# Kernel tuning notes

Measured on AMD Instinct MI355X. Metric: run time of the kernel, lower is better.

## Reference

```python
import jax, jax.numpy as jnp
import numpy as np

N = 16383        # complete binary tree, 14 levels
D_NODE = 512
D_SSM = 512
D_STATE = 16
MAX_DEPTH = 14   # number of BFS levels (depth 0..13)
LN_EPS = 1e-5


def setup_inputs() -> dict:
    key = jax.random.key(0)
    ks = jax.random.split(key, 8)
    # tree structure: parent[i] = (i-1)//2, root has parent -1; BFS order == index order
    parent = np.concatenate([np.array([-1]), (np.arange(1, N) - 1) // 2]).astype(np.int64)
    depth = np.floor(np.log2(np.arange(N) + 1)).astype(np.int32)
    s = jax.random.normal(ks[0], (N, D_NODE), jnp.float32)
    w = jax.random.uniform(ks[1], (N,), jnp.float32, minval=0.01, maxval=1.0)
    # parameters (xavier-ish scales)
    W_in = jax.random.normal(ks[2], (D_SSM, D_NODE + 1), jnp.float32) * (1.0 / np.sqrt(D_NODE + 1))
    b_in = jnp.zeros((D_SSM,), jnp.float32)
    W_delta = jax.random.normal(ks[3], (D_SSM, D_SSM), jnp.float32) * (1.0 / np.sqrt(D_SSM))
    # dt-style bias init: softplus(b) ~ dt in [1e-3, 1e-1]
    dt = jnp.exp(jax.random.uniform(ks[4], (D_SSM,), jnp.float32) * (np.log(0.1) - np.log(0.001)) + np.log(0.001))
    b_delta = dt + jnp.log(-jnp.expm1(-dt))
    W_w = jax.random.normal(ks[5], (D_SSM, 1), jnp.float32)
    b_w = jnp.zeros((D_SSM,), jnp.float32)
    A_log = jnp.log(jnp.broadcast_to(jnp.arange(1.0, D_STATE + 1.0, dtype=jnp.float32)[None, :], (D_SSM, D_STATE)))
    D = jnp.ones((D_SSM,), jnp.float32)
    W_B = jax.random.normal(ks[6], (D_STATE, D_SSM), jnp.float32) * (1.0 / np.sqrt(D_SSM))
    b_B = jnp.zeros((D_STATE,), jnp.float32)
    W_C = jax.random.normal(ks[7], (D_STATE, D_SSM), jnp.float32) * (1.0 / np.sqrt(D_SSM))
    b_C = jnp.zeros((D_STATE,), jnp.float32)
    gamma = jnp.ones((D_SSM,), jnp.float32)
    beta = jnp.zeros((D_SSM,), jnp.float32)
    return {"s": s, "w": w, "parent": jnp.asarray(parent), "depth": jnp.asarray(depth),
            "W_in": W_in, "b_in": b_in, "W_delta": W_delta, "b_delta": b_delta,
            "W_w": W_w, "b_w": b_w, "A_log": A_log, "D": D,
            "W_B": W_B, "b_B": b_B, "W_C": W_C, "b_C": b_C,
            "gamma": gamma, "beta": beta}


def reference(s, w, parent, depth, W_in, b_in, W_delta, b_delta, W_w, b_w,
              A_log, D, W_B, b_B, W_C, b_C, gamma, beta):
    n = s.shape[0]
    log_w = jnp.log(w + 1e-6)[:, None]                       # [N, 1]
    feat = jnp.concatenate([s, log_w], axis=1)               # [N, d_node+1]
    x = feat @ W_in.T + b_in                                 # [N, d_ssm]
    delta = jax.nn.softplus(x @ W_delta.T + b_delta) * jax.nn.sigmoid(log_w @ W_w.T + b_w)  # [N, d_ssm]
    A = -jnp.exp(A_log)                                      # [d_ssm, d_state]
    B = x @ W_B.T + b_B                                      # [N, d_state]
    C = x @ W_C.T + b_C                                      # [N, d_state]
    A_bar = jnp.exp(delta[:, :, None] * A[None])             # [N, d_ssm, d_state]
    Bx = (delta * x)[:, :, None] * B[:, None, :]             # [N, d_ssm, d_state]
    # level-parallel tree scan: all nodes at BFS depth l updated together
    par = jnp.maximum(parent, 0)
    has_par = (parent >= 0)[:, None, None]
    H = jnp.zeros((n, A_bar.shape[1], A_bar.shape[2]), x.dtype)
    for lvl in range(MAX_DEPTH):
        h_par = jnp.where(has_par, jnp.take(H, par, axis=0), 0.0)
        H = jnp.where((depth == lvl)[:, None, None], A_bar * h_par + Bx, H)
    Y = jnp.einsum('nds,ns->nd', H, C) + D * x               # [N, d_ssm]
    mu = jnp.mean(Y, axis=-1, keepdims=True)
    var = jnp.var(Y, axis=-1, keepdims=True)
    return (Y - mu) / jnp.sqrt(var + LN_EPS) * gamma + beta
```

## Files before the change

### kernel.cpp

```cpp
#include <hip/hip_runtime.h>
#include <hip/hip_bf16.h>
#include <math.h>

#define D_SSM 512
#define D_STATE 16
#define CKPT_BASE 511
#define CKPT_END 1023
#define N_CKPT 512
#define MPAD 16384

typedef __attribute__((ext_vector_type(8))) short short8;
typedef __attribute__((ext_vector_type(4))) float floatx4;

__device__ __forceinline__ unsigned short f2bf(float f) {
    unsigned int u = __float_as_uint(f);
    unsigned int r = (u + 0x7fffu + ((u >> 16) & 1u)) >> 16;
    return (unsigned short)r;
}
__device__ __forceinline__ float bf2f(unsigned short u) {
    return __uint_as_float(((unsigned int)u) << 16);
}
__device__ __forceinline__ void g2lds16(const void* g, void* l) {
    __builtin_amdgcn_global_load_lds(
        (const __attribute__((address_space(1))) void*)g,
        (__attribute__((address_space(3))) void*)l, 16, 0, 0);
}

__global__ __launch_bounds__(256) void prep_kernel(
    const float* __restrict__ s, const float* __restrict__ w,
    const float* __restrict__ W_in, const float* __restrict__ W_delta,
    const float* __restrict__ W_B, const float* __restrict__ W_C,
    unsigned short* __restrict__ s_bf, float* __restrict__ lw,
    unsigned short* __restrict__ Win_bf, unsigned short* __restrict__ Wd_bf,
    unsigned short* __restrict__ Wbc_bf, int Nn)
{
    const int b = blockIdx.x, t = threadIdx.x;
    if (b < MPAD) {
        unsigned int pack = 0;
        if (b < Nn) {
            float2 sv = *(const float2*)(s + (size_t)b * 512 + t * 2);
            pack = (unsigned int)f2bf(sv.x) | ((unsigned int)f2bf(sv.y) << 16);
        }
        *(unsigned int*)(s_bf + (size_t)b * 512 + t * 2) = pack;
        if (t == 0) lw[b] = (b < Nn) ? logf(w[b] + 1e-6f) : 0.f;
    } else if (b < MPAD + 512) {
        int c = b - MPAD;
        float a0 = W_in[(size_t)c * 513 + t * 2];
        float a1 = W_in[(size_t)c * 513 + t * 2 + 1];
        *(unsigned int*)(Win_bf + (size_t)c * 512 + t * 2) =
            (unsigned int)f2bf(a0) | ((unsigned int)f2bf(a1) << 16);
    } else if (b < MPAD + 1024) {
        int c = b - MPAD - 512;
        float2 wv = *(const float2*)(W_delta + (size_t)c * 512 + t * 2);
        *(unsigned int*)(Wd_bf + (size_t)c * 512 + t * 2) =
            (unsigned int)f2bf(wv.x) | ((unsigned int)f2bf(wv.y) << 16);
    } else {
        int c = b - MPAD - 1024;
        const float* src = (c < 16) ? (W_B + (size_t)c * 512) : (W_C + (size_t)(c - 16) * 512);
        float2 wv = *(const float2*)(src + t * 2);
        *(unsigned int*)(Wbc_bf + (size_t)c * 512 + t * 2) =
            (unsigned int)f2bf(wv.x) | ((unsigned int)f2bf(wv.y) << 16);
    }
}

__global__ __launch_bounds__(256) void gemm_mfma(
    const unsigned short* __restrict__ Abf,
    const unsigned short* __restrict__ Wbf,
    float* __restrict__ outf,
    unsigned short* __restrict__ outbf,
    const float* __restrict__ bias,
    const float* __restrict__ lw,
    const float* __restrict__ wcol, int wcol_stride,
    const float* __restrict__ bw,
    int mode)
{
    __shared__ __align__(16) short As[2][64 * 32];
    __shared__ __align__(16) short Bs[2][128 * 32];
    const int tid = threadIdx.x;
    const int wave = tid >> 6, lane = tid & 63;
    const int row0 = blockIdx.y * 64;
    const int col0 = blockIdx.x * 128;
    const int wr = (wave >> 1) * 32;
    const int wc = (wave & 1) * 64;

    floatx4 acc[2][4] = {};

    const int srow = lane >> 2;
    const int sg   = (lane & 3) ^ ((srow >> 1) & 3);
    const int scol = sg * 8;

    const unsigned short* Ag = Abf + (size_t)(row0 + wave * 16 + srow) * 512 + scol;
    const unsigned short* Wg0 = Wbf + (size_t)(col0 + (wave * 2 + 0) * 16 + srow) * 512 + scol;
    const unsigned short* Wg1 = Wbf + (size_t)(col0 + (wave * 2 + 1) * 16 + srow) * 512 + scol;

    {
        g2lds16(Ag, (char*)&As[0][0] + wave * 1024);
        g2lds16(Wg0, (char*)&Bs[0][0] + (wave * 2 + 0) * 1024);
        g2lds16(Wg1, (char*)&Bs[0][0] + (wave * 2 + 1) * 1024);
    }
    __syncthreads();

    for (int it = 0; it < 16; it++) {
        const int cur = it & 1;
        if (it < 15) {
            int k1 = (it + 1) * 32;
            g2lds16(Ag + k1, (char*)&As[cur ^ 1][0] + wave * 1024);
            g2lds16(Wg0 + k1, (char*)&Bs[cur ^ 1][0] + (wave * 2 + 0) * 1024);
            g2lds16(Wg1 + k1, (char*)&Bs[cur ^ 1][0] + (wave * 2 + 1) * 1024);
        }

        short8 af[2], bfr[4];
        #pragma unroll
        for (int i = 0; i < 2; i++) {
            int m = wr + i * 16 + (lane & 15);
            int gm = (lane >> 4) ^ ((m >> 1) & 3);
            af[i] = *(const short8*)&As[cur][m * 32 + gm * 8];
        }
        #pragma unroll
        for (int j = 0; j < 4; j++) {
            int n = wc + j * 16 + (lane & 15);
            int gn = (lane >> 4) ^ ((n >> 1) & 3);
            bfr[j] = *(const short8*)&Bs[cur][n * 32 + gn * 8];
        }
        #pragma unroll
        for (int i = 0; i < 2; i++)
            #pragma unroll
            for (int j = 0; j < 4; j++)
                acc[i][j] = __builtin_amdgcn_mfma_f32_16x16x32_bf16(af[i], bfr[j], acc[i][j], 0, 0, 0);
        __syncthreads();
    }

    #pragma unroll
    for (int i = 0; i < 2; i++) {
        #pragma unroll
        for (int reg = 0; reg < 4; reg++) {
            int r = row0 + wr + i * 16 + (lane >> 4) * 4 + reg;
            float lwr = lw[r];
            #pragma unroll
            for (int j = 0; j < 4; j++) {
                int c = col0 + wc + j * 16 + (lane & 15);
                float z = acc[i][j][reg] + bias[c];
                if (mode == 0) {
                    float o = z + lwr * wcol[(size_t)c * wcol_stride];
                    outbf[(size_t)r * 512 + c] = f2bf(o);
                } else {
                    float sp = (z > 15.f) ? z : log1pf(__expf(z));
                    float sg2 = 1.f / (1.f + __expf(-(lwr * wcol[c] + bw[c])));
                    outf[(size_t)r * 512 + c] = sp * sg2;
                }
            }
        }
    }
}

__global__ __launch_bounds__(256) void bc_gemm(
    const unsigned short* __restrict__ Abf,
    const unsigned short* __restrict__ Wbc,
    const float* __restrict__ b_B, const float* __restrict__ b_C,
    float* __restrict__ Bm, float* __restrict__ Cm)
{
    __shared__ __align__(16) short As[128 * 32];
    __shared__ __align__(16) short Ws[32 * 512];
    const int tid = threadIdx.x;
    const int wave = tid >> 6, lane = tid & 63;
    const int row0 = blockIdx.x * 128;
    const int wr = wave * 32;

    for (int i = 0; i < 8; i++) {
        int fg = i * 256 + tid;
        int n = fg >> 6, kgg = fg & 63;
        short8 v = *(const short8*)(Wbc + (size_t)n * 512 + kgg * 8);
        *(short8*)&Ws[n * 512 + ((kgg ^ (n & 7)) * 8)] = v;
    }

    floatx4 acc[2][2] = {};

    const int srow = lane >> 2;
    const int sgz  = (lane & 3) ^ ((srow >> 1) & 3);
    const int scol = sgz * 8;

    for (int k0 = 0; k0 < 512; k0 += 32) {
        #pragma unroll
        for (int j = 0; j < 2; j++) {
            int c = wave * 2 + j;
            int r = c * 16 + srow;
            g2lds16(Abf + (size_t)(row0 + r) * 512 + k0 + scol, (char*)As + c * 1024);
        }
        __syncthreads();

        short8 af[2], bfr[2];
        #pragma unroll
        for (int i = 0; i < 2; i++) {
            int m = wr + i * 16 + (lane & 15);
            int gm = (lane >> 4) ^ ((m >> 1) & 3);
            af[i] = *(const short8*)&As[m * 32 + gm * 8];
        }
        #pragma unroll
        for (int j = 0; j < 2; j++) {
            int n = j * 16 + (lane & 15);
            int Gg = (k0 >> 3) + (lane >> 4);
            bfr[j] = *(const short8*)&Ws[n * 512 + ((Gg ^ (n & 7)) * 8)];
        }
        #pragma unroll
        for (int i = 0; i < 2; i++)
            #pragma unroll
            for (int j = 0; j < 2; j++)
                acc[i][j] = __builtin_amdgcn_mfma_f32_16x16x32_bf16(af[i], bfr[j], acc[i][j], 0, 0, 0);
        __syncthreads();
    }

    const int s = lane & 15;
    #pragma unroll
    for (int i = 0; i < 2; i++) {
        #pragma unroll
        for (int reg = 0; reg < 4; reg++) {
            int r = row0 + wr + i * 16 + (lane >> 4) * 4 + reg;
            Bm[(size_t)r * 16 + s] = acc[i][0][reg] + b_B[s];
            Cm[(size_t)r * 16 + s] = acc[i][1][reg] + b_C[s];
        }
    }
}

__device__ __forceinline__ bool geo_check(const float* As) {
    bool ok = true;
    #pragma unroll
    for (int s = 1; s < 16; s++) {
        float want = (float)(s + 1) * As[0];
        ok = ok && (fabsf(As[s] - want) <= 1e-4f * (float)(s + 1));
    }
    return ok;
}

__global__ __launch_bounds__(256) void ckpt_kernel(
    const unsigned short* __restrict__ x_bf, const float* __restrict__ delta,
    const float* __restrict__ Bm, const float* __restrict__ A_log,
    float* __restrict__ H9)
{
    const int n9 = blockIdx.x;
    const int t = threadIdx.x;
    const int d0 = t, d1 = t + 256;

    float As0[16], As1[16], acc0[16], acc1[16];
    #pragma unroll
    for (int s = 0; s < 16; s++) {
        As0[s] = -__expf(A_log[d0 * 16 + s]);
        As1[s] = -__expf(A_log[d1 * 16 + s]);
        acc0[s] = 0.f; acc1[s] = 0.f;
    }
    const bool fast = geo_check(As0) && geo_check(As1);

    float cum0 = 0.f, cum1 = 0.f;
    int a = CKPT_BASE + n9;
    while (a >= 0) {
        float da0 = delta[(size_t)a * 512 + d0];
        float da1 = delta[(size_t)a * 512 + d1];
        float bx0 = da0 * bf2f(x_bf[(size_t)a * 512 + d0]);
        float bx1 = da1 * bf2f(x_bf[(size_t)a * 512 + d1]);
        if (fast) {
            float r0 = __expf(As0[0] * cum0);
            float r1 = __expf(As1[0] * cum1);
            float pw0 = r0, pw1 = r1;
            #pragma unroll
            for (int s = 0; s < 16; s++) {
                float Bs = Bm[a * 16 + s];
                acc0[s] = fmaf(bx0 * pw0, Bs, acc0[s]);
                acc1[s] = fmaf(bx1 * pw1, Bs, acc1[s]);
                pw0 *= r0; pw1 *= r1;
            }
        } else {
            #pragma unroll
            for (int s = 0; s < 16; s++) {
                float Bs = Bm[a * 16 + s];
                acc0[s] = fmaf(bx0 * __expf(As0[s] * cum0), Bs, acc0[s]);
                acc1[s] = fmaf(bx1 * __expf(As1[s] * cum1), Bs, acc1[s]);
            }
        }
        cum0 += da0; cum1 += da1;
        a = (a - 1) >> 1;
    }

    float* p0 = H9 + ((size_t)n9 * 512 + d0) * 16;
    float* p1 = H9 + ((size_t)n9 * 512 + d1) * 16;
    #pragma unroll
    for (int s = 0; s < 16; s++) { p0[s] = acc0[s]; p1[s] = acc1[s]; }
}

__global__ __launch_bounds__(256) void scan_shallow(
    const unsigned short* __restrict__ x_bf, const float* __restrict__ delta,
    const float* __restrict__ Bm, const float* __restrict__ Cm,
    const float* __restrict__ A_log, const float* __restrict__ Dv,
    const float* __restrict__ gamma, const float* __restrict__ beta,
    float* __restrict__ out)
{
    const int n = blockIdx.x;
    const int t = threadIdx.x;
    const int d0 = t, d1 = t + 256;

    float As0[16], As1[16], acc0[16], acc1[16];
    #pragma unroll
    for (int s = 0; s < 16; s++) {
        As0[s] = -__expf(A_log[d0 * 16 + s]);
        As1[s] = -__expf(A_log[d1 * 16 + s]);
        acc0[s] = 0.f; acc1[s] = 0.f;
    }
    const bool fast = geo_check(As0) && geo_check(As1);

    float cum0 = 0.f, cum1 = 0.f;
    int a = n;
    while (a >= 0) {
        float da0 = delta[(size_t)a * 512 + d0];
        float da1 = delta[(size_t)a * 512 + d1];
        float bx0 = da0 * bf2f(x_bf[(size_t)a * 512 + d0]);
        float bx1 = da1 * bf2f(x_bf[(size_t)a * 512 + d1]);
        if (fast) {
            float r0 = __expf(As0[0] * cum0);
            float r1 = __expf(As1[0] * cum1);
            float pw0 = r0, pw1 = r1;
            #pragma unroll
            for (int s = 0; s < 16; s++) {
                float Bs = Bm[a * 16 + s];
                acc0[s] = fmaf(bx0 * pw0, Bs, acc0[s]);
                acc1[s] = fmaf(bx1 * pw1, Bs, acc1[s]);
                pw0 *= r0; pw1 *= r1;
            }
        } else {
            #pragma unroll
            for (int s = 0; s < 16; s++) {
                float Bs = Bm[a * 16 + s];
                acc0[s] = fmaf(bx0 * __expf(As0[s] * cum0), Bs, acc0[s]);
                acc1[s] = fmaf(bx1 * __expf(As1[s] * cum1), Bs, acc1[s]);
            }
        }
        cum0 += da0; cum1 += da1;
        a = (a - 1) >> 1;
    }

    float xn0 = bf2f(x_bf[(size_t)n * 512 + d0]);
    float xn1 = bf2f(x_bf[(size_t)n * 512 + d1]);
    float y0 = Dv[d0] * xn0, y1 = Dv[d1] * xn1;
    #pragma unroll
    for (int s = 0; s < 16; s++) {
        float Cs = Cm[(size_t)n * 16 + s];
        y0 += Cs * acc0[s];
        y1 += Cs * acc1[s];
    }

    float s1 = y0 + y1;
    float s2 = y0 * y0 + y1 * y1;
    #pragma unroll
    for (int off = 32; off > 0; off >>= 1) {
        s1 += __shfl_xor(s1, off);
        s2 += __shfl_xor(s2, off);
    }
    __shared__ float red[8];
    int wid = t >> 6, lane = t & 63;
    if (lane == 0) { red[wid] = s1; red[wid + 4] = s2; }
    __syncthreads();
    float S1 = red[0] + red[1] + red[2] + red[3];
    float S2 = red[4] + red[5] + red[6] + red[7];
    float mu = S1 * (1.f / 512.f);
    float var = S2 * (1.f / 512.f) - mu * mu;
    float inv = rsqrtf(var + 1e-5f);
    out[(size_t)n * 512 + d0] = (y0 - mu) * inv * gamma[d0] + beta[d0];
    out[(size_t)n * 512 + d1] = (y1 - mu) * inv * gamma[d1] + beta[d1];
}

__global__ __launch_bounds__(512) void scan_deep(
    const unsigned short* __restrict__ x_bf, const float* __restrict__ delta,
    const float* __restrict__ Bm, const float* __restrict__ Cm,
    const float* __restrict__ H9,
    const float* __restrict__ A_log, const float* __restrict__ Dv,
    const float* __restrict__ gamma, const float* __restrict__ beta,
    float* __restrict__ out)
{
    __shared__ float Y[31][512];
    __shared__ int nid[31];
    const int p = blockIdx.x;
    const int d = threadIdx.x;
    const int a9 = CKPT_BASE + p;

    float As0 = -__expf(A_log[d * 16]);
    bool fast = true;
    #pragma unroll
    for (int s = 1; s < 16; s++) {
        float As = -__expf(A_log[d * 16 + s]);
        fast = fast && (fabsf(As - (float)(s + 1) * As0) <= 1e-4f * (float)(s + 1));
    }

    float H9v[16];
    #pragma unroll
    for (int s = 0; s < 16; s++) H9v[s] = H9[((size_t)p * 512 + d) * 16 + s];

    {
        float xv = bf2f(x_bf[(size_t)a9 * 512 + d]);
        float y = Dv[d] * xv;
        #pragma unroll
        for (int s = 0; s < 16; s++) y = fmaf(Cm[(size_t)a9 * 16 + s], H9v[s], y);
        Y[0][d] = y;
        if (d == 0) nid[0] = a9;
    }

    auto step = [&](int n, const float* Hp, float* Hc, int slot) {
        float dlt = delta[(size_t)n * 512 + d];
        float xv = bf2f(x_bf[(size_t)n * 512 + d]);
        float bx = dlt * xv;
        const float* Bn = Bm + (size_t)n * 16;
        const float* Cn = Cm + (size_t)n * 16;
        float y = Dv[d] * xv;
        if (fast) {
            float r = __expf(As0 * dlt);
            float pw = r;
            #pragma unroll
            for (int s = 0; s < 16; s++) {
                Hc[s] = fmaf(pw, Hp[s], bx * Bn[s]);
                y = fmaf(Cn[s], Hc[s], y);
                pw *= r;
            }
        } else {
            #pragma unroll
            for (int s = 0; s < 16; s++) {
                float Ab = __expf(dlt * (-__expf(A_log[d * 16 + s])));
                Hc[s] = fmaf(Ab, Hp[s], bx * Bn[s]);
                y = fmaf(Cn[s], Hc[s], y);
            }
        }
        Y[slot][d] = y;
        if (d == 0) nid[slot] = n;
    };

    float H10[16], H11[16], H12[16], H13[16];
    int slot = 1;
    #pragma unroll
    for (int c0 = 0; c0 < 2; c0++) {
        int n10 = 2 * a9 + 1 + c0;
        step(n10, H9v, H10, slot++);
        #pragma unroll
        for (int c1 = 0; c1 < 2; c1++) {
            int n11 = 2 * n10 + 1 + c1;
            step(n11, H10, H11, slot++);
            #pragma unroll
            for (int c2 = 0; c2 < 2; c2++) {
                int n12 = 2 * n11 + 1 + c2;
                step(n12, H11, H12, slot++);
                #pragma unroll
                for (int c3 = 0; c3 < 2; c3++) {
                    int n13 = 2 * n12 + 1 + c3;
                    step(n13, H12, H13, slot++);
                }
            }
        }
    }
    __syncthreads();

    const int w = d >> 6, lane = d & 63;
    for (int i = w; i < 31; i += 8) {
        int n = nid[i];
        float v[8]; float s1 = 0.f, s2 = 0.f;
        #pragma unroll
        for (int k = 0; k < 8; k++) {
            v[k] = Y[i][lane + 64 * k];
            s1 += v[k]; s2 += v[k] * v[k];
        }
        #pragma unroll
        for (int off = 32; off > 0; off >>= 1) {
            s1 += __shfl_xor(s1, off);
            s2 += __shfl_xor(s2, off);
        }
        float mu = s1 * (1.f / 512.f);
        float inv = rsqrtf(s2 * (1.f / 512.f) - mu * mu + 1e-5f);
        #pragma unroll
        for (int k = 0; k < 8; k++) {
            int ch = lane + 64 * k;
            out[(size_t)n * 512 + ch] = (v[k] - mu) * inv * gamma[ch] + beta[ch];
        }
    }
}

extern "C" void kernel_launch(void* const* d_in, const int* in_sizes, int n_in,
                              void* d_out, int out_size, void* d_ws, size_t ws_size,
                              hipStream_t stream) {
    const float* s_in   = (const float*)d_in[0];
    const float* w      = (const float*)d_in[1];
    const float* W_in    = (const float*)d_in[4];
    const float* b_in    = (const float*)d_in[5];
    const float* W_delta = (const float*)d_in[6];
    const float* b_delta = (const float*)d_in[7];
    const float* W_w     = (const float*)d_in[8];
    const float* b_w     = (const float*)d_in[9];
    const float* A_log   = (const float*)d_in[10];
    const float* Dv      = (const float*)d_in[11];
    const float* W_B     = (const float*)d_in[12];
    const float* b_B     = (const float*)d_in[13];
    const float* W_C     = (const float*)d_in[14];
    const float* b_C     = (const float*)d_in[15];
    const float* gamma   = (const float*)d_in[16];
    const float* beta    = (const float*)d_in[17];
    float* out = (float*)d_out;

    const int Nn = in_sizes[1];

    float* ws    = (float*)d_ws;
    float* lw    = ws;
    float* delta = lw + MPAD;
    float* Bm    = delta + (size_t)MPAD * 512;
    float* Cm    = Bm + (size_t)MPAD * 16;
    float* H9    = Cm + (size_t)MPAD * 16;
    unsigned short* s_bf  = (unsigned short*)(H9 + (size_t)N_CKPT * 512 * 16);
    unsigned short* x_bf  = s_bf + (size_t)MPAD * 512;
    unsigned short* Win_bf = x_bf + (size_t)MPAD * 512;
    unsigned short* Wd_bf  = Win_bf + 512 * 512;
    unsigned short* Wbc_bf = Wd_bf + 512 * 512;

    prep_kernel<<<MPAD + 1024 + 32, 256, 0, stream>>>(s_in, w, W_in, W_delta, W_B, W_C,
                                                      s_bf, lw, Win_bf, Wd_bf, Wbc_bf, Nn);

    dim3 gg(4, 256);
    gemm_mfma<<<gg, 256, 0, stream>>>(s_bf, Win_bf, nullptr, x_bf,
                                      b_in, lw, W_in + 512, 513, nullptr, 0);
    gemm_mfma<<<gg, 256, 0, stream>>>(x_bf, Wd_bf, delta, nullptr,
                                      b_delta, lw, W_w, 1, b_w, 1);

    bc_gemm<<<128, 256, 0, stream>>>(x_bf, Wbc_bf, b_B, b_C, Bm, Cm);

    ckpt_kernel<<<N_CKPT, 256, 0, stream>>>(x_bf, delta, Bm, A_log, H9);

    scan_shallow<<<CKPT_BASE, 256, 0, stream>>>(x_bf, delta, Bm, Cm, A_log, Dv,
                                                gamma, beta, out);

    scan_deep<<<N_CKPT, 512, 0, stream>>>(x_bf, delta, Bm, Cm, H9, A_log, Dv,
                                          gamma, beta, out);
}
```

Before: 264.6 us.

## Fuse B/C projection into delta GEMM and triple-buffer GEMM LDS pipeline

Removes the separate bc_gemm kernel by appending the W_B/W_C rows, zero-padded to 128, to the W_delta bf16 weight buffer. The delta GEMM gets a fifth column block whose epilogue writes Bm and Cm. The GEMM main loop moves from double to triple buffering, with explicit vmcnt waits and one barrier per iteration, to overlap global-to-LDS loads with MFMA. This cuts one launch and one re-read of x, at the cost of 96 wasted padded columns of MFMA work and more LDS per block.

```diff
diff --git a/kernel.cpp b/kernel.cpp
--- a/kernel.cpp
+++ b/kernel.cpp
@@ -32,7 +32,7 @@
     const float* __restrict__ W_B, const float* __restrict__ W_C,
     unsigned short* __restrict__ s_bf, float* __restrict__ lw,
     unsigned short* __restrict__ Win_bf, unsigned short* __restrict__ Wd_bf,
-    unsigned short* __restrict__ Wbc_bf, int Nn)
+    int Nn)
 {
     const int b = blockIdx.x, t = threadIdx.x;
     if (b < MPAD) {
@@ -56,9 +56,10 @@
             (unsigned int)f2bf(wv.x) | ((unsigned int)f2bf(wv.y) << 16);
     } else {
         int c = b - MPAD - 1024;
-        const float* src = (c < 16) ? (W_B + (size_t)c * 512) : (W_C + (size_t)(c - 16) * 512);
-        float2 wv = *(const float2*)(src + t * 2);
-        *(unsigned int*)(Wbc_bf + (size_t)c * 512 + t * 2) =
+        float2 wv; wv.x = 0.f; wv.y = 0.f;
+        if (c < 16)      wv = *(const float2*)(W_B + (size_t)c * 512 + t * 2);
+        else if (c < 32) wv = *(const float2*)(W_C + (size_t)(c - 16) * 512 + t * 2);
+        *(unsigned int*)(Wd_bf + (size_t)(512 + c) * 512 + t * 2) =
             (unsigned int)f2bf(wv.x) | ((unsigned int)f2bf(wv.y) << 16);
     }
 }
@@ -72,10 +73,12 @@
     const float* __restrict__ lw,
     const float* __restrict__ wcol, int wcol_stride,
     const float* __restrict__ bw,
+    const float* __restrict__ b_B, const float* __restrict__ b_C,
+    float* __restrict__ Bm, float* __restrict__ Cm,
     int mode)
 {
-    __shared__ __align__(16) short As[2][64 * 32];
-    __shared__ __align__(16) short Bs[2][128 * 32];
+    __shared__ __align__(16) short As[3][64 * 32];
+    __shared__ __align__(16) short Bs[3][128 * 32];
     const int tid = threadIdx.x;
     const int wave = tid >> 6, lane = tid & 63;
     const int row0 = blockIdx.y * 64;
@@ -89,26 +92,35 @@
     const int sg   = (lane & 3) ^ ((srow >> 1) & 3);
     const int scol = sg * 8;
 
-    const unsigned short* Ag = Abf + (size_t)(row0 + wave * 16 + srow) * 512 + scol;
+    const unsigned short* Ag  = Abf + (size_t)(row0 + wave * 16 + srow) * 512 + scol;
     const unsigned short* Wg0 = Wbf + (size_t)(col0 + (wave * 2 + 0) * 16 + srow) * 512 + scol;
     const unsigned short* Wg1 = Wbf + (size_t)(col0 + (wave * 2 + 1) * 16 + srow) * 512 + scol;
 
-    {
-        g2lds16(Ag, (char*)&As[0][0] + wave * 1024);
-        g2lds16(Wg0, (char*)&Bs[0][0] + (wave * 2 + 0) * 1024);
-        g2lds16(Wg1, (char*)&Bs[0][0] + (wave * 2 + 1) * 1024);
-    }
-    __syncthreads();
-
-    for (int it = 0; it < 16; it++) {
-        const int cur = it & 1;
-        if (it < 15) {
-            int k1 = (it + 1) * 32;
-            g2lds16(Ag + k1, (char*)&As[cur ^ 1][0] + wave * 1024);
-            g2lds16(Wg0 + k1, (char*)&Bs[cur ^ 1][0] + (wave * 2 + 0) * 1024);
-            g2lds16(Wg1 + k1, (char*)&Bs[cur ^ 1][0] + (wave * 2 + 1) * 1024);
-        }
-
+    char* Al  = (char*)&As[0][0] + wave * 1024;
+    char* Bl0 = (char*)&Bs[0][0] + (wave * 2 + 0) * 1024;
+    char* Bl1 = (char*)&Bs[0][0] + (wave * 2 + 1) * 1024;
+
+    #pragma unroll
+    for (int p = 0; p < 2; ++p) {
+        g2lds16(Ag  + p * 32, Al  + p * 4096);
+        g2lds16(Wg0 + p * 32, Bl0 + p * 8192);
+        g2lds16(Wg1 + p * 32, Bl1 + p * 8192);
+    }
+
+    #pragma unroll
+    for (int it = 0; it < 16; ++it) {
+        if (it < 15) asm volatile("s_waitcnt vmcnt(3)" ::: "memory");
+        else         asm volatile("s_waitcnt vmcnt(0)" ::: "memory");
+        __builtin_amdgcn_s_barrier();
+        __builtin_amdgcn_sched_barrier(0);
+        if (it < 14) {
+            const int nb = (it + 2) % 3;
+            const int k1 = (it + 2) * 32;
+            g2lds16(Ag  + k1, Al  + nb * 4096);
+            g2lds16(Wg0 + k1, Bl0 + nb * 8192);
+            g2lds16(Wg1 + k1, Bl1 + nb * 8192);
+        }
+        const int cur = it % 3;
         short8 af[2], bfr[4];
         #pragma unroll
         for (int i = 0; i < 2; i++) {
@@ -127,7 +139,24 @@
             #pragma unroll
             for (int j = 0; j < 4; j++)
                 acc[i][j] = __builtin_amdgcn_mfma_f32_16x16x32_bf16(af[i], bfr[j], acc[i][j], 0, 0, 0);
-        __syncthreads();
+    }
+
+    if (col0 >= 512) {
+        #pragma unroll
+        for (int i = 0; i < 2; i++) {
+            #pragma unroll
+            for (int reg = 0; reg < 4; reg++) {
+                int r = row0 + wr + i * 16 + (lane >> 4) * 4 + reg;
+                #pragma unroll
+                for (int j = 0; j < 4; j++) {
+                    int c2 = wc + j * 16 + (lane & 15);
+                    float z = acc[i][j][reg];
+                    if (c2 < 16)      Bm[(size_t)r * 16 + c2]        = z + b_B[c2];
+                    else if (c2 < 32) Cm[(size_t)r * 16 + (c2 - 16)] = z + b_C[c2 - 16];
+                }
+            }
+        }
+        return;
     }
 
     #pragma unroll
@@ -149,74 +178,6 @@
                     outf[(size_t)r * 512 + c] = sp * sg2;
                 }
             }
-        }
-    }
-}
-
-__global__ __launch_bounds__(256) void bc_gemm(
-    const unsigned short* __restrict__ Abf,
-    const unsigned short* __restrict__ Wbc,
-    const float* __restrict__ b_B, const float* __restrict__ b_C,
-    float* __restrict__ Bm, float* __restrict__ Cm)
-{
-    __shared__ __align__(16) short As[128 * 32];
-    __shared__ __align__(16) short Ws[32 * 512];
-    const int tid = threadIdx.x;
-    const int wave = tid >> 6, lane = tid & 63;
-    const int row0 = blockIdx.x * 128;
-    const int wr = wave * 32;
-
-    for (int i = 0; i < 8; i++) {
-        int fg = i * 256 + tid;
-        int n = fg >> 6, kgg = fg & 63;
-        short8 v = *(const short8*)(Wbc + (size_t)n * 512 + kgg * 8);
-        *(short8*)&Ws[n * 512 + ((kgg ^ (n & 7)) * 8)] = v;
-    }
-
-    floatx4 acc[2][2] = {};
-
-    const int srow = lane >> 2;
-    const int sgz  = (lane & 3) ^ ((srow >> 1) & 3);
-    const int scol = sgz * 8;
-
-    for (int k0 = 0; k0 < 512; k0 += 32) {
-        #pragma unroll
-        for (int j = 0; j < 2; j++) {
-            int c = wave * 2 + j;
-            int r = c * 16 + srow;
-            g2lds16(Abf + (size_t)(row0 + r) * 512 + k0 + scol, (char*)As + c * 1024);
-        }
-        __syncthreads();
-
-        short8 af[2], bfr[2];
-        #pragma unroll
-        for (int i = 0; i < 2; i++) {
-            int m = wr + i * 16 + (lane & 15);
-            int gm = (lane >> 4) ^ ((m >> 1) & 3);
-            af[i] = *(const short8*)&As[m * 32 + gm * 8];
-        }
-        #pragma unroll
-        for (int j = 0; j < 2; j++) {
-            int n = j * 16 + (lane & 15);
-            int Gg = (k0 >> 3) + (lane >> 4);
-            bfr[j] = *(const short8*)&Ws[n * 512 + ((Gg ^ (n & 7)) * 8)];
-        }
-        #pragma unroll
-        for (int i = 0; i < 2; i++)
-            #pragma unroll
-            for (int j = 0; j < 2; j++)
-                acc[i][j] = __builtin_amdgcn_mfma_f32_16x16x32_bf16(af[i], bfr[j], acc[i][j], 0, 0, 0);
-        __syncthreads();
-    }
-
-    const int s = lane & 15;
-    #pragma unroll
-    for (int i = 0; i < 2; i++) {
-        #pragma unroll
-        for (int reg = 0; reg < 4; reg++) {
-            int r = row0 + wr + i * 16 + (lane >> 4) * 4 + reg;
-            Bm[(size_t)r * 16 + s] = acc[i][0][reg] + b_B[s];
-            Cm[(size_t)r * 16 + s] = acc[i][1][reg] + b_C[s];
         }
     }
 }
@@ -509,18 +470,18 @@
     unsigned short* x_bf  = s_bf + (size_t)MPAD * 512;
     unsigned short* Win_bf = x_bf + (size_t)MPAD * 512;
     unsigned short* Wd_bf  = Win_bf + 512 * 512;
-    unsigned short* Wbc_bf = Wd_bf + 512 * 512;
-
-    prep_kernel<<<MPAD + 1024 + 32, 256, 0, stream>>>(s_in, w, W_in, W_delta, W_B, W_C,
-                                                      s_bf, lw, Win_bf, Wd_bf, Wbc_bf, Nn);
-
-    dim3 gg(4, 256);
-    gemm_mfma<<<gg, 256, 0, stream>>>(s_bf, Win_bf, nullptr, x_bf,
-                                      b_in, lw, W_in + 512, 513, nullptr, 0);
-    gemm_mfma<<<gg, 256, 0, stream>>>(x_bf, Wd_bf, delta, nullptr,
-                                      b_delta, lw, W_w, 1, b_w, 1);
-
-    bc_gemm<<<128, 256, 0, stream>>>(x_bf, Wbc_bf, b_B, b_C, Bm, Cm);
+
+    prep_kernel<<<MPAD + 1024 + 128, 256, 0, stream>>>(s_in, w, W_in, W_delta, W_B, W_C,
+                                                       s_bf, lw, Win_bf, Wd_bf, Nn);
+
+    dim3 g1(4, 256);
+    gemm_mfma<<<g1, 256, 0, stream>>>(s_bf, Win_bf, nullptr, x_bf,
+                                      b_in, lw, W_in + 512, 513, nullptr,
+                                      nullptr, nullptr, nullptr, nullptr, 0);
+    dim3 g2(5, 256);
+    gemm_mfma<<<g2, 256, 0, stream>>>(x_bf, Wd_bf, delta, nullptr,
+                                      b_delta, lw, W_w, 1, b_w,
+                                      b_B, b_C, Bm, Cm, 1);
 
     ckpt_kernel<<<N_CKPT, 256, 0, stream>>>(x_bf, delta, Bm, A_log, H9);
 
```

After: 266.7 us. No clear change (+0.8%).
